# Optimization experiments

Measured on AMD Instinct MI355X. Metric: run time of the kernel, lower is better.

## Reference

```python
import jax, jax.numpy as jnp
import numpy as np

N = 50000      # nodes per side
E = 800000     # edges per side
G = 1024       # graphs per batch
VOCAB = 100000
EMB, GH, EH, OUT = 128, 256, 256, 128
HID = GH + EH


def setup_inputs() -> dict:
    key = jax.random.key(0)
    ks = jax.random.split(key, 32)

    def xav(k, shape):
        lim = float(np.sqrt(6.0 / (shape[0] + shape[1])))
        return jax.random.uniform(k, shape, jnp.float32, -lim, lim)

    inp = {
        "x1": jax.random.randint(ks[0], (N,), 0, 11),
        "edge_index1": jax.random.randint(ks[1], (2, E), 0, N),
        "ent1": jax.random.randint(ks[2], (G,), 0, VOCAB),
        "batch1": jnp.sort(jax.random.randint(ks[3], (N,), 0, G)),
        "x2": jax.random.randint(ks[4], (N,), 0, 11),
        "edge_index2": jax.random.randint(ks[5], (2, E), 0, N),
        "ent2": jax.random.randint(ks[6], (G,), 0, VOCAB),
        "batch2": jnp.sort(jax.random.randint(ks[7], (N,), 0, G)),
        # shared GCN params (xavier weights, zero biases as in _reset_params)
        "atom_emb": xav(ks[8], (11, EMB)),
        "gW1": xav(ks[9], (EMB, GH)), "gb1": jnp.zeros((GH,), jnp.float32),
        "gW2": xav(ks[10], (GH, GH)), "gb2": jnp.zeros((GH,), jnp.float32),
        "fcW": xav(ks[11], (GH, GH)), "fcb": jnp.zeros((GH,), jnp.float32),
        # shared entity encoder params
        "ent_emb": xav(ks[12], (VOCAB, EMB)),
        "eW1": xav(ks[13], (EMB, EH)), "eb1": jnp.zeros((EH,), jnp.float32),
        "eW2": xav(ks[14], (EH, EH)), "eb2": jnp.zeros((EH,), jnp.float32),
        # decoder params
        "dW1": xav(ks[15], (HID, HID)), "db1": jnp.zeros((HID,), jnp.float32),
        "dW2": xav(ks[16], (HID, HID)), "db2": jnp.zeros((HID,), jnp.float32),
        "dW3": xav(ks[17], (HID, OUT)), "db3": jnp.zeros((OUT,), jnp.float32),
    }
    return inp


def _gcn_conv(x, W, b, src, dst, n):
    # PyG GCNConv: self-loops + symmetric normalization, out[dst] += norm * (x@W)[src]
    h = x @ W                                   # [n, d_out]
    loop = jnp.arange(n)
    s = jnp.concatenate([src, loop])
    d = jnp.concatenate([dst, loop])
    deg = jax.ops.segment_sum(jnp.ones_like(s, h.dtype), d, num_segments=n)
    dinv = jnp.where(deg > 0, jax.lax.rsqrt(jnp.maximum(deg, 1e-12)), 0.0)
    norm = dinv[s] * dinv[d]                    # [E+n]
    out = jax.ops.segment_sum(h[s] * norm[:, None], d, num_segments=n)
    return out + b


def _gcn_branch(x, edge_index, batch, atom_emb, gW1, gb1, gW2, gb2, fcW, fcb):
    src, dst = edge_index[0], edge_index[1]
    h = atom_emb[x]                             # [N, EMB]
    h = jax.nn.relu(_gcn_conv(h, gW1, gb1, src, dst, N))
    h = jax.nn.relu(_gcn_conv(h, gW2, gb2, src, dst, N))
    # global mean pool per graph
    counts = jax.ops.segment_sum(jnp.ones((N,), h.dtype), batch, num_segments=G)
    pooled = jax.ops.segment_sum(h, batch, num_segments=G) / jnp.maximum(counts, 1.0)[:, None]
    return pooled @ fcW + fcb                   # [G, GH]


def _enc(ent, ent_emb, eW1, eb1, eW2, eb2):
    e = jax.nn.relu(ent_emb[ent])
    e = jax.nn.relu(e @ eW1 + eb1)
    return jax.nn.relu(e @ eW2 + eb2)           # [G, EH]


def reference(x1, edge_index1, ent1, batch1, x2, edge_index2, ent2, batch2,
              atom_emb, gW1, gb1, gW2, gb2, fcW, fcb,
              ent_emb, eW1, eb1, eW2, eb2,
              dW1, db1, dW2, db2, dW3, db3):
    g1 = _gcn_branch(x1, edge_index1, batch1, atom_emb, gW1, gb1, gW2, gb2, fcW, fcb)
    g2 = _gcn_branch(x2, edge_index2, batch2, atom_emb, gW1, gb1, gW2, gb2, fcW, fcb)
    e1 = _enc(ent1, ent_emb, eW1, eb1, eW2, eb2)
    e2 = _enc(ent2, ent_emb, eW1, eb1, eW2, eb2)
    eg1 = jnp.concatenate([g1, e1], axis=1)     # [G, GH+EH]
    eg2 = jnp.concatenate([g2, e2], axis=1)
    egs = jax.nn.relu(eg1 + eg2)
    h = jax.nn.relu(egs @ dW1 + db1)
    h = jax.nn.relu(h @ dW2 + db2)
    return h @ dW3 + db3                        # [G, OUT]
```

## Files before the change

### kernel.cpp

```cpp
#include <hip/hip_runtime.h>
#include <hip/hip_fp16.h>

static constexpr int kN = 50000;
static constexpr int kE = 800000;
static constexpr int kG = 1024;
static constexpr int kEMB = 128;
static constexpr int kGH = 256;
static constexpr int kEH = 256;
static constexpr int kOUT = 128;
static constexpr int kHID = 512;
static constexpr int kNB = (kN + 255) / 256;
static constexpr int kMD = 64;
static constexpr int kNBKT = 196;
static constexpr int kEPB = 3125;
static constexpr int kPBLK = 256;
static constexpr int kPP = 8;

typedef __attribute__((ext_vector_type(8))) _Float16 half8v;
typedef __attribute__((ext_vector_type(4))) _Float16 half4v;
typedef __attribute__((ext_vector_type(4))) float floatx4;
typedef __attribute__((ext_vector_type(2))) float floatx2;


#define HS_SCALE 128.0f
#define HS_INV   (1.0f / 128.0f)

__device__ inline void acc_fp8x4(unsigned int w, float& a0, float& a1, float& a2, float& a3) {
    floatx2 lo = __builtin_amdgcn_cvt_pk_f32_fp8(w, false);
    floatx2 hi = __builtin_amdgcn_cvt_pk_f32_fp8(w, true);
    a0 += lo[0]; a1 += lo[1]; a2 += hi[0]; a3 += hi[1];
}

__device__ inline float grp16_reduce(float v) {
    int x;
    x = __builtin_amdgcn_update_dpp(0, __float_as_int(v), 0x121, 0xF, 0xF, true);
    v += __int_as_float(x);
    x = __builtin_amdgcn_update_dpp(0, __float_as_int(v), 0x122, 0xF, 0xF, true);
    v += __int_as_float(x);
    x = __builtin_amdgcn_update_dpp(0, __float_as_int(v), 0x124, 0xF, 0xF, true);
    v += __int_as_float(x);
    x = __builtin_amdgcn_update_dpp(0, __float_as_int(v), 0x128, 0xF, 0xF, true);
    v += __int_as_float(x);
    return v;
}

__global__ void prep_kernel(const float* __restrict__ atom_emb, const float* __restrict__ gW1,
                            const float* __restrict__ gW2,
                            float* __restrict__ M11, _Float16* __restrict__ w2t) {
    int i = blockIdx.x * 256 + threadIdx.x;
    if (blockIdx.x < 256) {
        int k = i >> 8, n = i & 255;
        w2t[(size_t)n * kGH + k] = (_Float16)gW2[(size_t)k * kGH + n];
    } else {
        int j = i - 65536;
        if (j < 11 * kGH) {
            int r = j >> 8, c = j & 255;
            float s = 0.f;
            for (int k = 0; k < kEMB; k++) s += atom_emb[r * kEMB + k] * gW1[k * kGH + c];
            M11[j] = s;
        }
    }
}

__global__ void wtrans_kernel(const float* __restrict__ dW1, const float* __restrict__ dW2,
                              const float* __restrict__ dW3, const float* __restrict__ fcW,
                              const float* __restrict__ eW1, const float* __restrict__ eW2,
                              _Float16* __restrict__ dW1t, _Float16* __restrict__ dW2t,
                              _Float16* __restrict__ dW3t, _Float16* __restrict__ fcWt,
                              _Float16* __restrict__ eW1t, _Float16* __restrict__ eW2t) {
    int b = blockIdx.x;
    const float* src; _Float16* dst; int K, N, j0;
    if (b < 1024)      { src = dW1; dst = dW1t; K = 512; N = 512; j0 = b * 256; }
    else if (b < 2048) { src = dW2; dst = dW2t; K = 512; N = 512; j0 = (b - 1024) * 256; }
    else if (b < 2304) { src = dW3; dst = dW3t; K = 512; N = 128; j0 = (b - 2048) * 256; }
    else if (b < 2560) { src = fcW; dst = fcWt; K = 256; N = 256; j0 = (b - 2304) * 256; }
    else if (b < 2688) { src = eW1; dst = eW1t; K = 128; N = 256; j0 = (b - 2560) * 256; }
    else               { src = eW2; dst = eW2t; K = 256; N = 256; j0 = (b - 2688) * 256; }
    int j = j0 + threadIdx.x;
    int n = j / K, k = j - n * K;
    dst[j] = (_Float16)src[(size_t)k * N + n];
}

__global__ void gbounds_kernel(const int* __restrict__ batch1, const int* __restrict__ batch2,
                               int* __restrict__ gstart) {
    int side = blockIdx.y;
    const int* batch = side ? batch2 : batch1;
    int g = blockIdx.x * 256 + threadIdx.x;
    if (g > kG) return;
    int lo = 0, hi = kN;
    while (lo < hi) { int mid = (lo + hi) >> 1; if (batch[mid] < g) lo = mid + 1; else hi = mid; }
    gstart[side * (kG + 1) + g] = lo;
}

__global__ void binp1_kernel(const int* __restrict__ ei1, const int* __restrict__ ei2,
                             int* __restrict__ poff) {
    int side = blockIdx.y;
    const int* dst = (side ? ei2 : ei1) + kE;
    __shared__ int hist[kNBKT];
    int t = threadIdx.x;
    if (t < kNBKT) hist[t] = 0;
    __syncthreads();
    int base = blockIdx.x * kEPB;
    for (int j = t; j < kEPB; j += 256)
        atomicAdd(&hist[dst[base + j] >> 8], 1);
    __syncthreads();
    if (t < kNBKT) poff[((side * kNBKT + t) << 8) | blockIdx.x] = hist[t];
}

__global__ void scanA_kernel(int* __restrict__ poff, int* __restrict__ btot) {
    int b = blockIdx.x, side = blockIdx.y, t = threadIdx.x;
    __shared__ int s[256];
    int idx = ((side * kNBKT + b) << 8) | t;
    int v = poff[idx];
    s[t] = v;
    __syncthreads();
    for (int o = 1; o < 256; o <<= 1) {
        int u = (t >= o) ? s[t - o] : 0;
        __syncthreads();
        s[t] += u;
        __syncthreads();
    }
    poff[idx] = s[t] - v;
    if (t == 255) btot[side * kNBKT + b] = s[255];
}

__global__ void scanB_kernel(const int* __restrict__ btot, int* __restrict__ bbase) {
    int side = blockIdx.x, t = threadIdx.x;
    __shared__ int s[256];
    int v = (t < kNBKT) ? btot[side * kNBKT + t] : 0;
    s[t] = v;
    __syncthreads();
    for (int o = 1; o < 256; o <<= 1) {
        int u = (t >= o) ? s[t - o] : 0;
        __syncthreads();
        s[t] += u;
        __syncthreads();
    }
    if (t < kNBKT) bbase[side * (kNBKT + 1) + t] = s[t] - v;
    if (t == 255) bbase[side * (kNBKT + 1) + kNBKT] = s[255];
}

__launch_bounds__(256)
__global__ void binp2_kernel(const int* __restrict__ ei1, const int* __restrict__ ei2,
                             const int* __restrict__ poff, const int* __restrict__ bbase,
                             unsigned int* __restrict__ ebuf) {
    int side = blockIdx.y, blk = blockIdx.x, t = threadIdx.x;
    const int* ei = side ? ei2 : ei1;
    __shared__ int hist[kNBKT], lb[kNBKT], gb[kNBKT], scanbuf[256];
    __shared__ unsigned int sorted[kEPB];
    if (t < kNBKT) hist[t] = 0;
    __syncthreads();
    int base = blk * kEPB;
    for (int j = t; j < kEPB; j += 256)
        atomicAdd(&hist[ei[kE + base + j] >> 8], 1);
    __syncthreads();
    int v = (t < kNBKT) ? hist[t] : 0;
    scanbuf[t] = v;
    __syncthreads();
    for (int o = 1; o < 256; o <<= 1) {
        int u = (t >= o) ? scanbuf[t - o] : 0;
        __syncthreads();
        scanbuf[t] += u;
        __syncthreads();
    }
    if (t < kNBKT) {
        lb[t] = scanbuf[t] - v;
        gb[t] = bbase[side * (kNBKT + 1) + t] + poff[((side * kNBKT + t) << 8) | blk];
        hist[t] = 0;
    }
    __syncthreads();
    for (int j = t; j < kEPB; j += 256) {
        int s_ = ei[base + j];
        int d  = ei[kE + base + j];
        int b  = d >> 8;
        int r  = atomicAdd(&hist[b], 1);
        sorted[lb[b] + r] = ((unsigned int)d << 16) | (unsigned int)s_;
    }
    __syncthreads();
    for (int j = t; j < kEPB; j += 256) {
        unsigned int val = sorted[j];
        int b = val >> 24;
        int gpos = gb[b] + (j - lb[b]);
        ebuf[(size_t)side * kE + gpos] = val;
    }
}

__global__ void binp3_kernel(const unsigned int* __restrict__ ebuf, const int* __restrict__ bbase,
                             unsigned short* __restrict__ col_ell, int* __restrict__ counts,
                             float* __restrict__ dinv, int2* __restrict__ xd,
                             const int* __restrict__ x1, const int* __restrict__ x2) {
    int b = blockIdx.x, side = blockIdx.y, t = threadIdx.x;
    __shared__ int cnt[256];
    cnt[t] = 0;
    __syncthreads();
    int start = bbase[side * (kNBKT + 1) + b];
    int end   = bbase[side * (kNBKT + 1) + b + 1];
    for (int k = start + t; k < end; k += 256) {
        unsigned int v = ebuf[(size_t)side * kE + k];
        int d8 = (v >> 16) & 255;
        int slot = atomicAdd(&cnt[d8], 1);
        if (slot > kMD - 1) slot = kMD - 1;
        int node = (b << 8) | d8;
        col_ell[((size_t)side * kN + node) * kMD + slot] = (unsigned short)(v & 0xFFFFu);
    }
    __syncthreads();
    int node = (b << 8) | t;
    if (node < kN) {
        int d = cnt[t];
        counts[side * kN + node] = d;
        float dv = rsqrtf((float)(d + 1));
        dinv[side * kN + node] = dv;
        const int* x = side ? x2 : x1;
        xd[side * kN + node] = make_int2(x[node], __float_as_int(dv));
    }
}

__global__ void conv1_combine_kernel(const int2* __restrict__ xd,
                                     const int* __restrict__ counts,
                                     const unsigned short* __restrict__ col_ell,
                                     const float* __restrict__ M11,
                                     const float* __restrict__ bias,
                                     _Float16* __restrict__ out) {
    int side = blockIdx.y;
    const int2* xdb = xd + (size_t)side * kN;
    const int* deg = counts + side * kN;
    const unsigned short* ci = col_ell + (size_t)side * kN * kMD;
    _Float16* ob = out + (size_t)side * kN * kGH;

    int tid = threadIdx.x;
    int sub = tid & 15;
    int v = blockIdx.x * 16 + (tid >> 4);

    int cnt = min(deg[v], kMD);
    const unsigned short* cv = ci + (size_t)v * kMD;
    float wt[11];
    #pragma unroll
    for (int t = 0; t < 11; t++) wt[t] = 0.f;
    for (int base = 0; base < cnt; base += 16) {
        int e = base + sub;
        int xs = 15; float ds = 0.f;
        if (e < cnt) {
            int2 t = xdb[(int)cv[e]];
            xs = t.x; ds = __int_as_float(t.y);
        }
        #pragma unroll
        for (int t = 0; t < 11; t++) wt[t] += (xs == t) ? ds : 0.f;
    }
    #pragma unroll
    for (int t = 0; t < 11; t++) wt[t] = grp16_reduce(wt[t]);

    int2 xv = xdb[v];
    float dv = __int_as_float(xv.y);
    #pragma unroll
    for (int q = 0; q < 4; q++) {
        int c = q * 64 + sub * 4;
        float4 bia = *(const float4*)(bias + c);
        float4 m = *(const float4*)(M11 + xv.x * kGH + c);
        float4 acc = make_float4(dv * m.x, dv * m.y, dv * m.z, dv * m.w);
        #pragma unroll
        for (int t = 0; t < 11; t++) {
            float w = wt[t];
            float4 mt = *(const float4*)(M11 + t * kGH + c);
            acc.x += w * mt.x; acc.y += w * mt.y;
            acc.z += w * mt.z; acc.w += w * mt.w;
        }
        half4v o;
        o[0] = (_Float16)fmaxf(dv * acc.x + bia.x, 0.f);
        o[1] = (_Float16)fmaxf(dv * acc.y + bia.y, 0.f);
        o[2] = (_Float16)fmaxf(dv * acc.z + bia.z, 0.f);
        o[3] = (_Float16)fmaxf(dv * acc.w + bia.w, 0.f);
        *(half4v*)(ob + (size_t)v * kGH + c) = o;
    }
}

__launch_bounds__(256)
__global__ void gemm2_mfma_kernel(const _Float16* __restrict__ A,
                                  const _Float16* __restrict__ Bt,
                                  const float* __restrict__ dinv,
                                  unsigned char* __restrict__ C) {
    __shared__ _Float16 As[128][72];
    __shared__ _Float16 Bs[128][72];

    int side = blockIdx.z;
    const _Float16* Ab = A + (size_t)side * kN * kGH;
    const float* db = dinv + (size_t)side * kN;
    unsigned char* Cb = C + (size_t)side * kN * kGH;

    int tid = threadIdx.x;
    int wave = tid >> 6, lane = tid & 63;
    int quad = lane >> 4, r = lane & 15;
    int wm = wave >> 1, wn = wave & 1;
    int row0 = blockIdx.x * 128;
    int col0 = blockIdx.y * 128;

    floatx4 acc[4][4];
    #pragma unroll
    for (int i = 0; i < 4; i++)
        #pragma unroll
        for (int j = 0; j < 4; j++) acc[i][j] = (floatx4){0.f, 0.f, 0.f, 0.f};

    for (int k0 = 0; k0 < kGH; k0 += 64) {
        #pragma unroll
        for (int u = 0; u < 4; u++) {
            int idx = tid + u * 256;
            int row = idx >> 3;
            int seg = (idx & 7) * 8;
            int gr = row0 + row;
            if (gr >= kN) gr = kN - 1;
            *(half8v*)&As[row][seg] = *(const half8v*)(Ab + (size_t)gr * kGH + k0 + seg);
            *(half8v*)&Bs[row][seg] = *(const half8v*)(Bt + (size_t)(col0 + row) * kGH + k0 + seg);
        }
        __syncthreads();
        #pragma unroll
        for (int ks = 0; ks < 2; ks++) {
            half8v af[4], bf[4];
            #pragma unroll
            for (int mt = 0; mt < 4; mt++)
                af[mt] = *(const half8v*)&As[wm * 64 + mt * 16 + r][ks * 32 + quad * 8];
            #pragma unroll
            for (int nt = 0; nt < 4; nt++)
                bf[nt] = *(const half8v*)&Bs[wn * 64 + nt * 16 + r][ks * 32 + quad * 8];
            #pragma unroll
            for (int mt = 0; mt < 4; mt++)
                #pragma unroll
                for (int nt = 0; nt < 4; nt++)
                    acc[mt][nt] = __builtin_amdgcn_mfma_f32_16x16x32_f16(af[mt], bf[nt],
                                                                         acc[mt][nt], 0, 0, 0);
        }
        __syncthreads();
    }

    #pragma unroll
    for (int mt = 0; mt < 4; mt++) {
        #pragma unroll
        for (int i = 0; i < 4; i++) {
            int grow = row0 + wm * 64 + mt * 16 + quad * 4 + i;
            if (grow >= kN) continue;
            float rsq = db[grow] * HS_SCALE;
            #pragma unroll
            for (int nt = 0; nt < 4; nt++) {
                int gcol = col0 + wn * 64 + nt * 16 + r;
                float q = acc[mt][nt][i] * rsq;
                Cb[(size_t)grow * kGH + gcol] =
                    (unsigned char)__builtin_amdgcn_cvt_pk_fp8_f32(q, q, 0, false);
            }
        }
    }
}

__launch_bounds__(256)
__global__ void gemm_tail_kernel(const _Float16* __restrict__ A,
                                 const _Float16* __restrict__ Bt,
                                 void* __restrict__ Cout,
                                 int N, int K,
                                 const float* __restrict__ bias,
                                 int relu, int f32out) {
    __shared__ _Float16 As[64][72];
    __shared__ _Float16 Bs[64][72];
    int tid = threadIdx.x;
    int wave = tid >> 6, lane = tid & 63;
    int quad = lane >> 4, r = lane & 15;
    int wm = wave >> 1, wn = wave & 1;
    int row0 = blockIdx.x * 64, col0 = blockIdx.y * 64;

    floatx4 acc[2][2];
    #pragma unroll
    for (int i = 0; i < 2; i++)
        #pragma unroll
        for (int j = 0; j < 2; j++) acc[i][j] = (floatx4){0.f, 0.f, 0.f, 0.f};

    for (int k0 = 0; k0 < K; k0 += 64) {
        #pragma unroll
        for (int u = 0; u < 2; u++) {
            int idx = tid + u * 256;
            int row = idx >> 3;
            int seg = (idx & 7) * 8;
            *(half8v*)&As[row][seg] = *(const half8v*)(A + (size_t)(row0 + row) * K + k0 + seg);
            *(half8v*)&Bs[row][seg] = *(const half8v*)(Bt + (size_t)(col0 + row) * K + k0 + seg);
        }
        __syncthreads();
        #pragma unroll
        for (int ks = 0; ks < 2; ks++) {
            half8v af[2], bf[2];
            #pragma unroll
            for (int mt = 0; mt < 2; mt++)
                af[mt] = *(const half8v*)&As[wm * 32 + mt * 16 + r][ks * 32 + quad * 8];
            #pragma unroll
            for (int nt = 0; nt < 2; nt++)
                bf[nt] = *(const half8v*)&Bs[wn * 32 + nt * 16 + r][ks * 32 + quad * 8];
            #pragma unroll
            for (int mt = 0; mt < 2; mt++)
                #pragma unroll
                for (int nt = 0; nt < 2; nt++)
                    acc[mt][nt] = __builtin_amdgcn_mfma_f32_16x16x32_f16(af[mt], bf[nt],
                                                                         acc[mt][nt], 0, 0, 0);
        }
        __syncthreads();
    }

    #pragma unroll
    for (int mt = 0; mt < 2; mt++) {
        #pragma unroll
        for (int i = 0; i < 4; i++) {
            int grow = row0 + wm * 32 + mt * 16 + quad * 4 + i;
            #pragma unroll
            for (int nt = 0; nt < 2; nt++) {
                int gcol = col0 + wn * 32 + nt * 16 + r;
                float v = acc[mt][nt][i] + bias[gcol];
                if (relu) v = fmaxf(v, 0.f);
                if (f32out) ((float*)Cout)[(size_t)grow * N + gcol] = v;
                else ((_Float16*)Cout)[(size_t)grow * N + gcol] = (_Float16)v;
            }
        }
    }
}

__global__ void aggpoolw_kernel(const unsigned char* __restrict__ hs, const float* __restrict__ dinv,
                                const int* __restrict__ counts,
                                const unsigned short* __restrict__ col_ell,
                                const float* __restrict__ bias,
                                const int* __restrict__ gstart,
                                float* __restrict__ ppart) {
    int side = blockIdx.y;
    int a = blockIdx.x * 4 + (threadIdx.x >> 6);
    int g = a >> 3;
    int pI = a & 7;
    const unsigned char* hb = hs + (size_t)side * kN * kGH;
    const float* dv_ = dinv + side * kN;
    const int* deg = counts + side * kN;
    const unsigned short* ci = col_ell + (size_t)side * kN * kMD;

    int start = gstart[side * (kG + 1) + g];
    int end   = gstart[side * (kG + 1) + g + 1];

    int lane = threadIdx.x & 63;
    int c = lane * 4;
    float4 bia = *(const float4*)(bias + c);
    float p0 = 0.f, p1 = 0.f, p2 = 0.f, p3 = 0.f;

    for (int v = start + pI; v < end; v += kPP) {
        float dv = dv_[v];
        float a0 = 0.f, a1 = 0.f, a2 = 0.f, a3 = 0.f;
        acc_fp8x4(*(const unsigned int*)(hb + (size_t)v * kGH + c), a0, a1, a2, a3);
        int cnt = min(deg[v], kMD);
        int idxl = (lane < cnt) ? (int)ci[(size_t)v * kMD + lane] : 0;
        int j = 0;
        for (; j + 16 <= cnt; j += 16) {
            unsigned int w[16];
            #pragma unroll
            for (int u = 0; u < 16; u++)
                w[u] = *(const unsigned int*)(hb + (size_t)__shfl(idxl, j + u) * kGH + c);
            #pragma unroll
            for (int u = 0; u < 16; u++) acc_fp8x4(w[u], a0, a1, a2, a3);
        }
        for (; j + 8 <= cnt; j += 8) {
            unsigned int w[8];
            #pragma unroll
            for (int u = 0; u < 8; u++)
                w[u] = *(const unsigned int*)(hb + (size_t)__shfl(idxl, j + u) * kGH + c);
            #pragma unroll
            for (int u = 0; u < 8; u++) acc_fp8x4(w[u], a0, a1, a2, a3);
        }
        for (; j < cnt; j++)
            acc_fp8x4(*(const unsigned int*)(hb + (size_t)__shfl(idxl, j) * kGH + c),
                      a0, a1, a2, a3);
        float f = dv * HS_INV;
        p0 += fmaxf(f * a0 + bia.x, 0.f);
        p1 += fmaxf(f * a1 + bia.y, 0.f);
        p2 += fmaxf(f * a2 + bia.z, 0.f);
        p3 += fmaxf(f * a3 + bia.w, 0.f);
    }

    *(float4*)(ppart + (((size_t)side * kG + g) * kPP + pI) * kGH + c) =
        make_float4(p0, p1, p2, p3);
}

__global__ void preduce_kernel(const float* __restrict__ ppart,
                               const int* __restrict__ gstart,
                               _Float16* __restrict__ pooled16) {
    int side = blockIdx.y;
    int g = blockIdx.x;
    int start = gstart[side * (kG + 1) + g];
    int end   = gstart[side * (kG + 1) + g + 1];
    int t = threadIdx.x;
    const float* pb = ppart + (((size_t)side * kG + g) * kPP) * kGH;
    float s = 0.f;
    #pragma unroll
    for (int p = 0; p < kPP; p++) s += pb[p * kGH + t];
    float inv = 1.0f / fmaxf((float)(end - start), 1.0f);
    pooled16[(size_t)(side * kG + g) * kGH + t] = (_Float16)(s * inv);
}

__global__ void egather_kernel(const float* __restrict__ emb,
                               const int* __restrict__ ent1, const int* __restrict__ ent2,
                               _Float16* __restrict__ e16) {
    int rr = blockIdx.x;
    int idx = (rr < kG) ? ent1[rr] : ent2[rr - kG];
    int k = threadIdx.x;
    e16[(size_t)rr * kEMB + k] = (_Float16)fmaxf(emb[(size_t)idx * kEMB + k], 0.f);
}

__global__ void egsprep_kernel(const _Float16* __restrict__ gfc16,
                               const _Float16* __restrict__ ento16,
                               _Float16* __restrict__ egs16) {
    int idx = blockIdx.x * 256 + threadIdx.x;
    int g = idx >> 6;
    int k8 = (idx & 63) * 8;
    const _Float16* src = (k8 < kGH) ? gfc16 : ento16;
    int kk = (k8 < kGH) ? k8 : k8 - kGH;
    half8v a = *(const half8v*)(src + (size_t)g * kGH + kk);
    half8v b = *(const half8v*)(src + (size_t)(g + kG) * kGH + kk);
    half8v o;
    #pragma unroll
    for (int u = 0; u < 8; u++) o[u] = (_Float16)fmaxf((float)a[u] + (float)b[u], 0.f);
    *(half8v*)(egs16 + (size_t)g * kHID + k8) = o;
}

static inline char* carve(char*& p, size_t bytes) {
    char* r = p;
    p += (bytes + 255) & ~(size_t)255;
    return r;
}

extern "C" void kernel_launch(void* const* d_in, const int* in_sizes, int n_in,
                              void* d_out, int out_size, void* d_ws, size_t ws_size,
                              hipStream_t stream) {
    const int*   x1       = (const int*)d_in[0];
    const int*   ei1      = (const int*)d_in[1];
    const int*   ent1     = (const int*)d_in[2];
    const int*   batch1   = (const int*)d_in[3];
    const int*   x2       = (const int*)d_in[4];
    const int*   ei2      = (const int*)d_in[5];
    const int*   ent2     = (const int*)d_in[6];
    const int*   batch2   = (const int*)d_in[7];
    const float* atom_emb = (const float*)d_in[8];
    const float* gW1      = (const float*)d_in[9];
    const float* gb1      = (const float*)d_in[10];
    const float* gW2      = (const float*)d_in[11];
    const float* gb2      = (const float*)d_in[12];
    const float* fcW      = (const float*)d_in[13];
    const float* fcb      = (const float*)d_in[14];
    const float* ent_emb  = (const float*)d_in[15];
    const float* eW1      = (const float*)d_in[16];
    const float* eb1      = (const float*)d_in[17];
    const float* eW2      = (const float*)d_in[18];
    const float* eb2      = (const float*)d_in[19];
    const float* dW1      = (const float*)d_in[20];
    const float* db1      = (const float*)d_in[21];
    const float* dW2      = (const float*)d_in[22];
    const float* db2      = (const float*)d_in[23];
    const float* dW3      = (const float*)d_in[24];
    const float* db3      = (const float*)d_in[25];
    float* out = (float*)d_out;

    char* p = (char*)d_ws;
    _Float16* h2_h   = (_Float16*)carve(p, (size_t)2 * kN * kGH * 2);
    unsigned char* hs8 = (unsigned char*)carve(p, (size_t)2 * kN * kGH);
    unsigned short* col_ell = (unsigned short*)carve(p, (size_t)2 * kN * kMD * 2);
    unsigned int* ebuf = (unsigned int*)carve(p, (size_t)2 * kE * 4);
    int*   poff    = (int*)  carve(p, (size_t)2 * kNBKT * 256 * 4);
    int*   btot    = (int*)  carve(p, (size_t)2 * kNBKT * 4);
    int*   bbase   = (int*)  carve(p, (size_t)2 * (kNBKT + 1) * 4);
    int*   counts  = (int*)  carve(p, (size_t)2 * kN * 4);
    float* dinv    = (float*)carve(p, (size_t)2 * kN * 4);
    int2*  xd      = (int2*) carve(p, (size_t)2 * kN * 8);
    int*   gstart  = (int*)  carve(p, (size_t)2 * (kG + 1) * 4);
    float* M11     = (float*)carve(p, 11 * kGH * 4);
    _Float16* w2t  = (_Float16*)carve(p, (size_t)kGH * kGH * 2);
    float* ppart   = (float*)carve(p, (size_t)2 * kG * kPP * kGH * 4);
    _Float16* pooled16 = (_Float16*)carve(p, (size_t)2 * kG * kGH * 2);
    _Float16* gfc16    = (_Float16*)carve(p, (size_t)2 * kG * kGH * 2);
    _Float16* e16      = (_Float16*)carve(p, (size_t)2 * kG * kEMB * 2);
    _Float16* etmp16   = (_Float16*)carve(p, (size_t)2 * kG * kEH * 2);
    _Float16* ento16   = (_Float16*)carve(p, (size_t)2 * kG * kEH * 2);
    _Float16* egs16    = (_Float16*)carve(p, (size_t)kG * kHID * 2);
    _Float16* dh1_16   = (_Float16*)carve(p, (size_t)kG * kHID * 2);
    _Float16* dh2_16   = (_Float16*)carve(p, (size_t)kG * kHID * 2);
    _Float16* dW1t = (_Float16*)carve(p, (size_t)kHID * kHID * 2);
    _Float16* dW2t = (_Float16*)carve(p, (size_t)kHID * kHID * 2);
    _Float16* dW3t = (_Float16*)carve(p, (size_t)kOUT * kHID * 2);
    _Float16* fcWt = (_Float16*)carve(p, (size_t)kGH * kGH * 2);
    _Float16* eW1t = (_Float16*)carve(p, (size_t)kEH * kEMB * 2);
    _Float16* eW2t = (_Float16*)carve(p, (size_t)kEH * kEH * 2);

    prep_kernel<<<267, 256, 0, stream>>>(atom_emb, gW1, gW2, M11, w2t);
    wtrans_kernel<<<2944, 256, 0, stream>>>(dW1, dW2, dW3, fcW, eW1, eW2,
                                            dW1t, dW2t, dW3t, fcWt, eW1t, eW2t);
    gbounds_kernel<<<dim3((kG + 256) / 256, 2), 256, 0, stream>>>(batch1, batch2, gstart);
    binp1_kernel<<<dim3(kPBLK, 2), 256, 0, stream>>>(ei1, ei2, poff);
    scanA_kernel<<<dim3(kNBKT, 2), 256, 0, stream>>>(poff, btot);
    scanB_kernel<<<2, 256, 0, stream>>>(btot, bbase);
    binp2_kernel<<<dim3(kPBLK, 2), 256, 0, stream>>>(ei1, ei2, poff, bbase, ebuf);
    binp3_kernel<<<dim3(kNBKT, 2), 256, 0, stream>>>(ebuf, bbase, col_ell, counts,
                                                     dinv, xd, x1, x2);
    conv1_combine_kernel<<<dim3(kN / 16, 2), 256, 0, stream>>>(xd, counts, col_ell,
                                                               M11, gb1, h2_h);

    gemm2_mfma_kernel<<<dim3((kN + 127) / 128, kGH / 128, 2), 256, 0, stream>>>(h2_h, w2t,
                                                                                dinv, hs8);
    aggpoolw_kernel<<<dim3(kG * kPP / 4, 2), 256, 0, stream>>>(hs8, dinv, counts, col_ell,
                                                               gb2, gstart, ppart);
    preduce_kernel<<<dim3(kG, 2), 256, 0, stream>>>(ppart, gstart, pooled16);
    egather_kernel<<<2 * kG, 128, 0, stream>>>(ent_emb, ent1, ent2, e16);

    gemm_tail_kernel<<<dim3(2 * kG / 64, kGH / 64), 256, 0, stream>>>(
        pooled16, fcWt, gfc16, kGH, kGH, fcb, 0, 0);
    gemm_tail_kernel<<<dim3(2 * kG / 64, kEH / 64), 256, 0, stream>>>(
        e16, eW1t, etmp16, kEH, kEMB, eb1, 1, 0);
    gemm_tail_kernel<<<dim3(2 * kG / 64, kEH / 64), 256, 0, stream>>>(
        etmp16, eW2t, ento16, kEH, kEH, eb2, 1, 0);
    egsprep_kernel<<<kG * kHID / 8 / 256, 256, 0, stream>>>(gfc16, ento16, egs16);
    gemm_tail_kernel<<<dim3(kG / 64, kHID / 64), 256, 0, stream>>>(
        egs16, dW1t, dh1_16, kHID, kHID, db1, 1, 0);
    gemm_tail_kernel<<<dim3(kG / 64, kHID / 64), 256, 0, stream>>>(
        dh1_16, dW2t, dh2_16, kHID, kHID, db2, 1, 0);
    gemm_tail_kernel<<<dim3(kG / 64, kOUT / 64), 256, 0, stream>>>(
        dh2_16, dW3t, out, kOUT, kHID, db3, 0, 1);
}
```

Measured before the change: 422.6 us.

## Move conv1 combine to an MFMA GEMM and split aggregate from pooling

The conv1 combine step now writes a small per-node fp16 weight vector of 32 entries. A separate MFMA GEMM multiplies it by a transposed fp16 copy of atom_emb@gW1, replacing the scalar FMA loop over 11 types per output column. Layer-2 aggregation is now one wave per node: it writes full fp16 node features, and a separate pool kernel sums them per graph. This replaces the fused per-graph aggregate-and-pool kernel with its partial buffers. The new path adds launches and extra global traffic: a write and re-read of 50k×256 fp16 per side, and the wt16 buffer. The split path also trades the per-graph load imbalance for that traffic, and reduces precision to fp16 for the M11 product.

```diff
diff --git a/kernel.cpp b/kernel.cpp
--- a/kernel.cpp
+++ b/kernel.cpp
@@ -14,7 +14,6 @@
 static constexpr int kNBKT = 196;
 static constexpr int kEPB = 3125;
 static constexpr int kPBLK = 256;
-static constexpr int kPP = 8;
 
 typedef __attribute__((ext_vector_type(8))) _Float16 half8v;
 typedef __attribute__((ext_vector_type(4))) _Float16 half4v;
@@ -46,7 +45,8 @@
 
 __global__ void prep_kernel(const float* __restrict__ atom_emb, const float* __restrict__ gW1,
                             const float* __restrict__ gW2,
-                            float* __restrict__ M11, _Float16* __restrict__ w2t) {
+                            float* __restrict__ M11, _Float16* __restrict__ w2t,
+                            _Float16* __restrict__ m11t) {
     int i = blockIdx.x * 256 + threadIdx.x;
     if (blockIdx.x < 256) {
         int k = i >> 8, n = i & 255;
@@ -58,6 +58,13 @@
             float s = 0.f;
             for (int k = 0; k < kEMB; k++) s += atom_emb[r * kEMB + k] * gW1[k * kGH + c];
             M11[j] = s;
+        } else if (j < 11 * kGH + 256 * 32) {
+            int j2 = j - 11 * kGH;
+            int n = j2 >> 5, k = j2 & 31;
+            float s = 0.f;
+            if (k < 11)
+                for (int p = 0; p < kEMB; p++) s += atom_emb[k * kEMB + p] * gW1[p * kGH + n];
+            m11t[j2] = (_Float16)s;
         }
     }
 }
@@ -215,17 +222,15 @@
     }
 }
 
-__global__ void conv1_combine_kernel(const int2* __restrict__ xd,
-                                     const int* __restrict__ counts,
-                                     const unsigned short* __restrict__ col_ell,
-                                     const float* __restrict__ M11,
-                                     const float* __restrict__ bias,
-                                     _Float16* __restrict__ out) {
+__global__ void conv1_wt_kernel(const int2* __restrict__ xd,
+                                const int* __restrict__ counts,
+                                const unsigned short* __restrict__ col_ell,
+                                _Float16* __restrict__ wt16) {
     int side = blockIdx.y;
     const int2* xdb = xd + (size_t)side * kN;
     const int* deg = counts + side * kN;
     const unsigned short* ci = col_ell + (size_t)side * kN * kMD;
-    _Float16* ob = out + (size_t)side * kN * kGH;
+    _Float16* wb = wt16 + (size_t)side * kN * 32;
 
     int tid = threadIdx.x;
     int sub = tid & 15;
@@ -251,25 +256,72 @@
 
     int2 xv = xdb[v];
     float dv = __int_as_float(xv.y);
-    #pragma unroll
-    for (int q = 0; q < 4; q++) {
-        int c = q * 64 + sub * 4;
-        float4 bia = *(const float4*)(bias + c);
-        float4 m = *(const float4*)(M11 + xv.x * kGH + c);
-        float4 acc = make_float4(dv * m.x, dv * m.y, dv * m.z, dv * m.w);
-        #pragma unroll
-        for (int t = 0; t < 11; t++) {
-            float w = wt[t];
-            float4 mt = *(const float4*)(M11 + t * kGH + c);
-            acc.x += w * mt.x; acc.y += w * mt.y;
-            acc.z += w * mt.z; acc.w += w * mt.w;
-        }
-        half4v o;
-        o[0] = (_Float16)fmaxf(dv * acc.x + bia.x, 0.f);
-        o[1] = (_Float16)fmaxf(dv * acc.y + bia.y, 0.f);
-        o[2] = (_Float16)fmaxf(dv * acc.z + bia.z, 0.f);
-        o[3] = (_Float16)fmaxf(dv * acc.w + bia.w, 0.f);
-        *(half4v*)(ob + (size_t)v * kGH + c) = o;
+    float dv2 = dv * dv;
+    float mywt = 0.f;
+    #pragma unroll
+    for (int t = 0; t < 11; t++) mywt = (sub == t) ? wt[t] : mywt;
+    float wp = dv * mywt + dv2 * ((xv.x == sub) ? 1.f : 0.f);
+    wb[(size_t)v * 32 + sub] = (_Float16)wp;
+    wb[(size_t)v * 32 + 16 + sub] = (_Float16)0.f;
+}
+
+__launch_bounds__(256)
+__global__ void gemm1_kernel(const _Float16* __restrict__ wt16,
+                             const _Float16* __restrict__ m11t,
+                             const float* __restrict__ bias,
+                             _Float16* __restrict__ h2) {
+    __shared__ _Float16 As[64][40];
+    __shared__ _Float16 Bs[64][40];
+    int side = blockIdx.z;
+    const _Float16* Ab = wt16 + (size_t)side * kN * 32;
+    _Float16* Ob = h2 + (size_t)side * kN * kGH;
+    int tid = threadIdx.x;
+    int wave = tid >> 6, lane = tid & 63;
+    int quad = lane >> 4, r = lane & 15;
+    int wm = wave >> 1, wn = wave & 1;
+    int row0 = blockIdx.x * 64, col0 = blockIdx.y * 64;
+
+    {
+        int row = tid >> 2, seg = (tid & 3) * 8;
+        int gr = row0 + row;
+        if (gr >= kN) gr = kN - 1;
+        *(half8v*)&As[row][seg] = *(const half8v*)(Ab + (size_t)gr * 32 + seg);
+        *(half8v*)&Bs[row][seg] = *(const half8v*)(m11t + (size_t)(col0 + row) * 32 + seg);
+    }
+    __syncthreads();
+
+    floatx4 acc[2][2];
+    #pragma unroll
+    for (int i = 0; i < 2; i++)
+        #pragma unroll
+        for (int j = 0; j < 2; j++) acc[i][j] = (floatx4){0.f, 0.f, 0.f, 0.f};
+    half8v af[2], bf[2];
+    #pragma unroll
+    for (int mt = 0; mt < 2; mt++)
+        af[mt] = *(const half8v*)&As[wm * 32 + mt * 16 + r][quad * 8];
+    #pragma unroll
+    for (int nt = 0; nt < 2; nt++)
+        bf[nt] = *(const half8v*)&Bs[wn * 32 + nt * 16 + r][quad * 8];
+    #pragma unroll
+    for (int mt = 0; mt < 2; mt++)
+        #pragma unroll
+        for (int nt = 0; nt < 2; nt++)
+            acc[mt][nt] = __builtin_amdgcn_mfma_f32_16x16x32_f16(af[mt], bf[nt],
+                                                                 acc[mt][nt], 0, 0, 0);
+
+    #pragma unroll
+    for (int mt = 0; mt < 2; mt++) {
+        #pragma unroll
+        for (int i = 0; i < 4; i++) {
+            int grow = row0 + wm * 32 + mt * 16 + quad * 4 + i;
+            if (grow >= kN) continue;
+            #pragma unroll
+            for (int nt = 0; nt < 2; nt++) {
+                int gcol = col0 + wn * 32 + nt * 16 + r;
+                float v = acc[mt][nt][i] + bias[gcol];
+                Ob[(size_t)grow * kGH + gcol] = (_Float16)fmaxf(v, 0.f);
+            }
+        }
     }
 }
 
@@ -415,78 +467,78 @@
     }
 }
 
-__global__ void aggpoolw_kernel(const unsigned char* __restrict__ hs, const float* __restrict__ dinv,
-                                const int* __restrict__ counts,
-                                const unsigned short* __restrict__ col_ell,
-                                const float* __restrict__ bias,
-                                const int* __restrict__ gstart,
-                                float* __restrict__ ppart) {
+__global__ void aggregate2_kernel(const unsigned char* __restrict__ hs, const float* __restrict__ dinv,
+                                  const int* __restrict__ counts,
+                                  const unsigned short* __restrict__ col_ell,
+                                  const float* __restrict__ bias, _Float16* __restrict__ out) {
     int side = blockIdx.y;
-    int a = blockIdx.x * 4 + (threadIdx.x >> 6);
-    int g = a >> 3;
-    int pI = a & 7;
     const unsigned char* hb = hs + (size_t)side * kN * kGH;
     const float* dv_ = dinv + side * kN;
     const int* deg = counts + side * kN;
     const unsigned short* ci = col_ell + (size_t)side * kN * kMD;
-
+    _Float16* ob = out + (size_t)side * kN * kGH;
+
+    int wave = threadIdx.x >> 6;
+    int lane = threadIdx.x & 63;
+    int v = blockIdx.x * 4 + wave;
+    if (v >= kN) return;
+    int c = lane * 4;
+    float4 bia = *(const float4*)(bias + c);
+    float dv = dv_[v];
+    float a0 = 0.f, a1 = 0.f, a2 = 0.f, a3 = 0.f;
+    acc_fp8x4(*(const unsigned int*)(hb + (size_t)v * kGH + c), a0, a1, a2, a3);
+    int cnt = min(deg[v], kMD);
+    int idxl = (lane < cnt) ? (int)ci[(size_t)v * kMD + lane] : 0;
+    int j = 0;
+    for (; j + 16 <= cnt; j += 16) {
+        unsigned int w[16];
+        #pragma unroll
+        for (int u = 0; u < 16; u++)
+            w[u] = *(const unsigned int*)(hb + (size_t)__shfl(idxl, j + u) * kGH + c);
+        #pragma unroll
+        for (int u = 0; u < 16; u++) acc_fp8x4(w[u], a0, a1, a2, a3);
+    }
+    for (; j + 8 <= cnt; j += 8) {
+        unsigned int w[8];
+        #pragma unroll
+        for (int u = 0; u < 8; u++)
+            w[u] = *(const unsigned int*)(hb + (size_t)__shfl(idxl, j + u) * kGH + c);
+        #pragma unroll
+        for (int u = 0; u < 8; u++) acc_fp8x4(w[u], a0, a1, a2, a3);
+    }
+    for (; j < cnt; j++)
+        acc_fp8x4(*(const unsigned int*)(hb + (size_t)__shfl(idxl, j) * kGH + c),
+                  a0, a1, a2, a3);
+    float f = dv * HS_INV;
+    half4v o;
+    o[0] = (_Float16)fmaxf(f * a0 + bia.x, 0.f);
+    o[1] = (_Float16)fmaxf(f * a1 + bia.y, 0.f);
+    o[2] = (_Float16)fmaxf(f * a2 + bia.z, 0.f);
+    o[3] = (_Float16)fmaxf(f * a3 + bia.w, 0.f);
+    __builtin_nontemporal_store(o, (half4v*)(ob + (size_t)v * kGH + c));
+}
+
+__global__ void poolfast_kernel(const _Float16* __restrict__ h,
+                                const int* __restrict__ gstart,
+                                _Float16* __restrict__ pooled16) {
+    int side = blockIdx.y;
+    int g = blockIdx.x;
+    const _Float16* hb = h + (size_t)side * kN * kGH;
     int start = gstart[side * (kG + 1) + g];
     int end   = gstart[side * (kG + 1) + g + 1];
-
-    int lane = threadIdx.x & 63;
+    int wave = threadIdx.x >> 6, lane = threadIdx.x & 63;
     int c = lane * 4;
-    float4 bia = *(const float4*)(bias + c);
-    float p0 = 0.f, p1 = 0.f, p2 = 0.f, p3 = 0.f;
-
-    for (int v = start + pI; v < end; v += kPP) {
-        float dv = dv_[v];
-        float a0 = 0.f, a1 = 0.f, a2 = 0.f, a3 = 0.f;
-        acc_fp8x4(*(const unsigned int*)(hb + (size_t)v * kGH + c), a0, a1, a2, a3);
-        int cnt = min(deg[v], kMD);
-        int idxl = (lane < cnt) ? (int)ci[(size_t)v * kMD + lane] : 0;
-        int j = 0;
-        for (; j + 16 <= cnt; j += 16) {
-            unsigned int w[16];
-            #pragma unroll
-            for (int u = 0; u < 16; u++)
-                w[u] = *(const unsigned int*)(hb + (size_t)__shfl(idxl, j + u) * kGH + c);
-            #pragma unroll
-            for (int u = 0; u < 16; u++) acc_fp8x4(w[u], a0, a1, a2, a3);
-        }
-        for (; j + 8 <= cnt; j += 8) {
-            unsigned int w[8];
-            #pragma unroll
-            for (int u = 0; u < 8; u++)
-                w[u] = *(const unsigned int*)(hb + (size_t)__shfl(idxl, j + u) * kGH + c);
-            #pragma unroll
-            for (int u = 0; u < 8; u++) acc_fp8x4(w[u], a0, a1, a2, a3);
-        }
-        for (; j < cnt; j++)
-            acc_fp8x4(*(const unsigned int*)(hb + (size_t)__shfl(idxl, j) * kGH + c),
-                      a0, a1, a2, a3);
-        float f = dv * HS_INV;
-        p0 += fmaxf(f * a0 + bia.x, 0.f);
-        p1 += fmaxf(f * a1 + bia.y, 0.f);
-        p2 += fmaxf(f * a2 + bia.z, 0.f);
-        p3 += fmaxf(f * a3 + bia.w, 0.f);
-    }
-
-    *(float4*)(ppart + (((size_t)side * kG + g) * kPP + pI) * kGH + c) =
-        make_float4(p0, p1, p2, p3);
-}
-
-__global__ void preduce_kernel(const float* __restrict__ ppart,
-                               const int* __restrict__ gstart,
-                               _Float16* __restrict__ pooled16) {
-    int side = blockIdx.y;
-    int g = blockIdx.x;
-    int start = gstart[side * (kG + 1) + g];
-    int end   = gstart[side * (kG + 1) + g + 1];
+    float a0 = 0.f, a1 = 0.f, a2 = 0.f, a3 = 0.f;
+    for (int v = start + wave; v < end; v += 4) {
+        half4v hv = *(const half4v*)(hb + (size_t)v * kGH + c);
+        a0 += (float)hv[0]; a1 += (float)hv[1];
+        a2 += (float)hv[2]; a3 += (float)hv[3];
+    }
+    __shared__ float ps[4][256];
+    *(float4*)&ps[wave][c] = make_float4(a0, a1, a2, a3);
+    __syncthreads();
     int t = threadIdx.x;
-    const float* pb = ppart + (((size_t)side * kG + g) * kPP) * kGH;
-    float s = 0.f;
-    #pragma unroll
-    for (int p = 0; p < kPP; p++) s += pb[p * kGH + t];
+    float s = ps[0][t] + ps[1][t] + ps[2][t] + ps[3][t];
     float inv = 1.0f / fmaxf((float)(end - start), 1.0f);
     pooled16[(size_t)(side * kG + g) * kGH + t] = (_Float16)(s * inv);
 }
@@ -567,7 +619,8 @@
     int*   gstart  = (int*)  carve(p, (size_t)2 * (kG + 1) * 4);
     float* M11     = (float*)carve(p, 11 * kGH * 4);
     _Float16* w2t  = (_Float16*)carve(p, (size_t)kGH * kGH * 2);
-    float* ppart   = (float*)carve(p, (size_t)2 * kG * kPP * kGH * 4);
+    _Float16* m11t = (_Float16*)carve(p, (size_t)256 * 32 * 2);
+    _Float16* wt16 = (_Float16*)carve(p, (size_t)2 * kN * 32 * 2);
     _Float16* pooled16 = (_Float16*)carve(p, (size_t)2 * kG * kGH * 2);
     _Float16* gfc16    = (_Float16*)carve(p, (size_t)2 * kG * kGH * 2);
     _Float16* e16      = (_Float16*)carve(p, (size_t)2 * kG * kEMB * 2);
@@ -583,7 +636,7 @@
     _Float16* eW1t = (_Float16*)carve(p, (size_t)kEH * kEMB * 2);
     _Float16* eW2t = (_Float16*)carve(p, (size_t)kEH * kEH * 2);
 
-    prep_kernel<<<267, 256, 0, stream>>>(atom_emb, gW1, gW2, M11, w2t);
+    prep_kernel<<<299, 256, 0, stream>>>(atom_emb, gW1, gW2, M11, w2t, m11t);
     wtrans_kernel<<<2944, 256, 0, stream>>>(dW1, dW2, dW3, fcW, eW1, eW2,
                                             dW1t, dW2t, dW3t, fcWt, eW1t, eW2t);
     gbounds_kernel<<<dim3((kG + 256) / 256, 2), 256, 0, stream>>>(batch1, batch2, gstart);
@@ -593,14 +646,14 @@
     binp2_kernel<<<dim3(kPBLK, 2), 256, 0, stream>>>(ei1, ei2, poff, bbase, ebuf);
     binp3_kernel<<<dim3(kNBKT, 2), 256, 0, stream>>>(ebuf, bbase, col_ell, counts,
                                                      dinv, xd, x1, x2);
-    conv1_combine_kernel<<<dim3(kN / 16, 2), 256, 0, stream>>>(xd, counts, col_ell,
-                                                               M11, gb1, h2_h);
-
+    conv1_wt_kernel<<<dim3(kN / 16, 2), 256, 0, stream>>>(xd, counts, col_ell, wt16);
+    gemm1_kernel<<<dim3((kN + 63) / 64, kGH / 64, 2), 256, 0, stream>>>(wt16, m11t,
+                                                                        gb1, h2_h);
     gemm2_mfma_kernel<<<dim3((kN + 127) / 128, kGH / 128, 2), 256, 0, stream>>>(h2_h, w2t,
                                                                                 dinv, hs8);
-    aggpoolw_kernel<<<dim3(kG * kPP / 4, 2), 256, 0, stream>>>(hs8, dinv, counts, col_ell,
-                                                               gb2, gstart, ppart);
-    preduce_kernel<<<dim3(kG, 2), 256, 0, stream>>>(ppart, gstart, pooled16);
+    aggregate2_kernel<<<dim3((kN + 3) / 4, 2), 256, 0, stream>>>(hs8, dinv, counts, col_ell,
+                                                                 gb2, h2_h);
+    poolfast_kernel<<<dim3(kG, 2), 256, 0, stream>>>(h2_h, gstart, pooled16);
     egather_kernel<<<2 * kG, 128, 0, stream>>>(ent_emb, ent1, ent2, e16);
 
     gemm_tail_kernel<<<dim3(2 * kG / 64, kGH / 64), 256, 0, stream>>>(
```

After: 398.1 us. -5.8%, faster.
